# Kernel tuning notes

Hardware: AMD Instinct MI355X
Metric: run time of the kernel (lower is better)

The kernel has to match this reference:

```python
import jax, jax.numpy as jnp
import numpy as np

B = 512; Nt = 8; Nr = 8; Ld = 256; Lp = 16; qAry = 2
LDPC_N = qAry * Nt * Ld      # 4096
M_A = 3 * LDPC_N             # 12288
SQ2 = float(np.sqrt(2.0))


def setup_inputs() -> dict:
    key = jax.random.key(0)
    ks = jax.random.split(key, 12)
    # Sparse-ish binary ADMM expansion matrix A (rows = check-edge constraints)
    A = (jax.random.uniform(ks[0], (M_A, LDPC_N)) < 0.005).astype(jnp.float32)
    # Lambda_A ~ column weights of A (keeps the w denominator well behaved)
    Lambda_A = (jnp.sum(A, axis=0) + 1.0).reshape(LDPC_N, 1)
    theta = jax.random.uniform(ks[1], (M_A, 1), dtype=jnp.float32)
    sigma2_I = jnp.tile(0.1 * jnp.eye(2 * Nt, dtype=jnp.float32)[None], (B, 1, 1))
    return {
        "sigma2_I": sigma2_I,
        "Y": jax.random.normal(ks[2], (B, 2 * Nr, Ld), dtype=jnp.float32),
        "YYp": jax.random.normal(ks[3], (B, Nr, 2 * (Ld + Lp)), dtype=jnp.float32),
        "real_Xp": jax.random.normal(ks[4], (B, Nt, Lp), dtype=jnp.float32) / SQ2,
        "imag_Xp": jax.random.normal(ks[5], (B, Nt, Lp), dtype=jnp.float32) / SQ2,
        "lambda_W": jax.random.uniform(ks[6], (B, 1, 1), minval=0.5, maxval=1.5),
        "F": jax.random.normal(ks[7], (B, 2 * Nt, Ld), dtype=jnp.float32),
        "u": jax.random.uniform(ks[8], (B, LDPC_N, 1), dtype=jnp.float32),
        "z": jax.random.uniform(ks[9], (B, M_A, 1), dtype=jnp.float32),
        "lambda1": jax.random.uniform(ks[10], (B, M_A, 1), dtype=jnp.float32),
        "acc_new": jnp.zeros((B, 1, 1), dtype=jnp.float32),
        "A": A, "theta": theta, "Lambda_A": Lambda_A,
        "miu": jnp.full((1, 1), 0.6, dtype=jnp.float32),
        "alpha": jnp.full((1, 1), 11.0, dtype=jnp.float32),
        "factor": jnp.full((1, 1), 1.0, dtype=jnp.float32),
        "relax": jnp.full((1, 1), 1.0, dtype=jnp.float32),
        "acc": jnp.full((1, 1), 0.0, dtype=jnp.float32),
    }


def reference(sigma2_I, Y, YYp, real_Xp, imag_Xp, lambda_W, F, u, z, lambda1,
              acc_new, A, theta, Lambda_A, miu, alpha, factor, relax, acc):
    relu = jax.nn.relu
    z_old, lam_old = z, lambda1
    A_T = A.T
    # --- qAry == 2 detection update ---
    fb = 4.0 * lambda_W                                   # (B,1,1)
    # reorder F (B, 2Nt, Ld) into bit layout (B, 2*Nt*Ld, 1)
    res = F.transpose(0, 2, 1).reshape(-1, Ld, 2, Nt).transpose(0, 1, 3, 2)
    res = res.reshape(-1, 2 * Nt * Ld, 1)
    fb_res = 2.0 * lambda_W - 2.0 * SQ2 * res
    q = miu * jnp.matmul(A_T, theta - z - lambda1) + fb_res - alpha  # (B,LDPC_N,1)
    w = 1.0 / (miu * Lambda_A + fb - 2.0 * alpha)
    u = q * w
    u = relu(u) - relu(u - 1.0)                           # clip to [0,1]
    u_order = u.reshape(-1, Ld, Nt, qAry).transpose(0, 2, 1, 3)  # (B,Nt,Ld,2)
    real_X = (1.0 - 2.0 * u_order[:, :, :, 0]) / SQ2      # (B,Nt,Ld)
    imag_X = (1.0 - 2.0 * u_order[:, :, :, 1]) / SQ2
    X = jnp.concatenate([real_X, imag_X], axis=1)          # (B,2Nt,Ld)
    # --- MMSE channel re-estimation ---
    real_XXp = jnp.concatenate([real_X, real_Xp], axis=2)
    imag_XXp = jnp.concatenate([imag_X, imag_Xp], axis=2)
    XXp = jnp.concatenate([jnp.concatenate([real_XXp, imag_XXp], 2),
                           jnp.concatenate([-imag_XXp, real_XXp], 2)], 1)  # (B,2Nt,2(Ld+Lp))
    R = jnp.matmul(XXp, XXp.transpose(0, 2, 1)) + sigma2_I  # (B,2Nt,2Nt)
    inv_R = jnp.linalg.inv(R)
    W_temp = jnp.matmul(jnp.matmul(inv_R, XXp), YYp.transpose(0, 2, 1))  # (B,2Nt,Nr)
    real_W = W_temp[:, :Nt, :]
    imag_W = W_temp[:, Nt:2 * Nt, :]
    W = jnp.concatenate([jnp.concatenate([real_W, imag_W], 2),
                         jnp.concatenate([-imag_W, real_W], 2)], 1).transpose(0, 2, 1)  # (B,2Nr,2Nt)
    lambda_W = factor * lambda_W
    WT = W.transpose(0, 2, 1)
    F_new = jnp.matmul(WT, Y) + lambda_W * X - jnp.matmul(jnp.matmul(WT, W), X)
    # --- z / lambda1 ADMM update ---
    ztemp = theta - relax * jnp.matmul(A, u) - (1.0 - relax) * (theta - z_old) - lambda1
    z = relu(ztemp)
    lambda1 = -ztemp + z
    z = z + acc * (z - z_old)
    lambda1 = lambda1 + acc * (lambda1 - lam_old)
    return (lambda_W, F_new, u, z, lambda1, acc_new)
```

## Files before the change

### kernel.cpp

```cpp
#include <hip/hip_runtime.h>
#include <math.h>

#define BB 512
#define NT 8
#define NR 8
#define LDIM 256
#define LP 16
#define LDPC_N 4096
#define M_A 12288
#define COLCAP 128
#define ROWCAP 64
#define K2I 16
#define SQ2 1.41421356237309515f
#define INVSQ2 0.70710678118654752f

typedef unsigned short u16;
typedef unsigned int u32;

__device__ __forceinline__ float bflo(u32 u) { return __uint_as_float(u << 16); }
__device__ __forceinline__ float bfhi(u32 u) { return __uint_as_float(u & 0xffff0000u); }
__device__ __forceinline__ u16 f2bf(float f) {
  u32 b = __float_as_uint(f);
  return (u16)((b + 0x7fffu + ((b >> 16) & 1u)) >> 16);
}

__global__ __launch_bounds__(256) void build_sparse(
    const float* __restrict__ A, int* __restrict__ colcnt, int* __restrict__ rowcnt,
    int* __restrict__ csc_c, int* __restrict__ csr_c) {
  const long long total4 = (long long)M_A * LDPC_N / 4;
  long long stride = (long long)gridDim.x * blockDim.x;
  for (long long t = (long long)blockIdx.x * blockDim.x + threadIdx.x; t < total4; t += stride) {
    float4 a = ((const float4*)A)[t];
    long long base = t * 4;
    float av[4] = {a.x, a.y, a.z, a.w};
#pragma unroll
    for (int l = 0; l < 4; l++) {
      if (av[l] != 0.0f) {
        long long lin = base + l;
        int i = (int)(lin >> 12);
        int j = (int)(lin & 4095);
        int sc = atomicAdd(&colcnt[j], 1);
        if (sc < COLCAP) csc_c[j * COLCAP + sc] = i;
        int sr = atomicAdd(&rowcnt[i], 1);
        if (sr < ROWCAP) csr_c[i * ROWCAP + sr] = j;
      }
    }
  }
}

__global__ __launch_bounds__(256) void t1tf(
    const float* __restrict__ z, const float* __restrict__ lam,
    const float* __restrict__ theta, const float* __restrict__ F,
    u16* __restrict__ VT, u16* __restrict__ FT) {
  __shared__ float tile[256 * 33];
  int bx = blockIdx.x;
  if (bx < 6144) {
    int i0 = (bx % 384) * 32, b0 = (bx / 384) * 32;
    {
      int il = threadIdx.x & 31, bq = threadIdx.x >> 5;
      float th = theta[i0 + il];
#pragma unroll
      for (int m = 0; m < 4; m++) {
        int bl = bq + m * 8;
        size_t off = (size_t)(b0 + bl) * M_A + i0 + il;
        tile[il * 33 + bl] = th - z[off] - lam[off];
      }
    }
    __syncthreads();
    {
      int bl = threadIdx.x & 31, iq = threadIdx.x >> 5;
#pragma unroll
      for (int m = 0; m < 4; m++) {
        int il = iq + m * 8;
        VT[(size_t)(i0 + il) * BB + b0 + bl] = f2bf(tile[il * 33 + bl]);
      }
    }
  } else {
    int t = bx - 6144;
    int j0 = (t & 15) * 256, b0 = (t >> 4) * 32;
    int ld0 = j0 >> 4;
    int cc = threadIdx.x >> 4, dd = threadIdx.x & 15;
    int jl = dd * 16 + ((cc & 7) << 1) + (cc >> 3);
    for (int m = 0; m < 32; m++) {
      tile[jl * 33 + m] = F[(size_t)(b0 + m) * 4096 + cc * 256 + ld0 + dd];
    }
    __syncthreads();
    int bl = threadIdx.x & 31, jq = threadIdx.x >> 5;
    for (int jj = 0; jj < 32; jj++) {
      int jlo = jq * 32 + jj;
      FT[(size_t)(j0 + jlo) * BB + b0 + bl] = f2bf(tile[jlo * 33 + bl]);
    }
  }
}

__global__ __launch_bounds__(256) void k1_spmm(
    const u16* __restrict__ VT, const u16* __restrict__ FT,
    const int* __restrict__ colcnt, const int* __restrict__ csc_c,
    const float* __restrict__ lambda_W, const float* __restrict__ Lambda_A,
    const float* __restrict__ miu_p, const float* __restrict__ alpha_p,
    u16* __restrict__ UT) {
  __shared__ int idx[4 * COLCAP];
  __shared__ int cnts[4];
  __shared__ float lamA[4];
  int j0 = blockIdx.x * 4;
  int t = threadIdx.x;
  for (int s = t; s < 4 * COLCAP; s += 256) idx[s] = csc_c[j0 * COLCAP + s];
  if (t < 4) {
    cnts[t] = min(colcnt[j0 + t], COLCAP);
    lamA[t] = Lambda_A[j0 + t];
  }
  __syncthreads();
  float miu = miu_p[0], alpha = alpha_p[0];
  float2 lw2 = *(const float2*)&lambda_W[2 * t];
#pragma unroll
  for (int c = 0; c < 4; c++) {
    int cnt = cnts[c];
    const int* ic = &idx[c * COLCAP];
    float a0 = 0.0f, a1 = 0.0f;
    int k = 0;
    for (; k + 3 < cnt; k += 4) {
      int4 i4 = *(const int4*)&ic[k];
      u32 w0 = *(const u32*)&VT[(size_t)i4.x * BB + 2 * t];
      u32 w1 = *(const u32*)&VT[(size_t)i4.y * BB + 2 * t];
      u32 w2 = *(const u32*)&VT[(size_t)i4.z * BB + 2 * t];
      u32 w3 = *(const u32*)&VT[(size_t)i4.w * BB + 2 * t];
      a0 += (bflo(w0) + bflo(w1)) + (bflo(w2) + bflo(w3));
      a1 += (bfhi(w0) + bfhi(w1)) + (bfhi(w2) + bfhi(w3));
    }
    for (; k < cnt; k++) {
      u32 w = *(const u32*)&VT[(size_t)ic[k] * BB + 2 * t];
      a0 += bflo(w);
      a1 += bfhi(w);
    }
    int j = j0 + c;
    u32 rr = *(const u32*)&FT[(size_t)j * BB + 2 * t];
    float res0 = bflo(rr), res1 = bfhi(rr);
    float q0 = miu * a0 + 2.0f * lw2.x - 2.0f * SQ2 * res0 - alpha;
    float q1 = miu * a1 + 2.0f * lw2.y - 2.0f * SQ2 * res1 - alpha;
    float w0 = 1.0f / (miu * lamA[c] + 4.0f * lw2.x - 2.0f * alpha);
    float w1 = 1.0f / (miu * lamA[c] + 4.0f * lw2.y - 2.0f * alpha);
    float u0 = fminf(fmaxf(q0 * w0, 0.0f), 1.0f);
    float u1 = fminf(fmaxf(q1 * w1, 0.0f), 1.0f);
    u32 packed = (u32)f2bf(u0) | ((u32)f2bf(u1) << 16);
    *(u32*)&UT[(size_t)j * BB + 2 * t] = packed;
  }
}

__global__ __launch_bounds__(256) void tu_ut(const u16* __restrict__ UT, float* __restrict__ out_u) {
  __shared__ float tile[32 * 33];
  int j0 = blockIdx.x * 32, b0 = blockIdx.y * 32;
  {
    int bl = threadIdx.x & 31, jq = threadIdx.x >> 5;
#pragma unroll
    for (int m = 0; m < 4; m++) {
      int jl = jq + m * 8;
      tile[jl * 33 + bl] = bflo((u32)UT[(size_t)(j0 + jl) * BB + b0 + bl]);
    }
  }
  __syncthreads();
  {
    int jl = threadIdx.x & 31, bq = threadIdx.x >> 5;
#pragma unroll
    for (int m = 0; m < 4; m++) {
      int bl = bq + m * 8;
      out_u[(size_t)(b0 + bl) * LDPC_N + j0 + jl] = tile[jl * 33 + bl];
    }
  }
}

__global__ __launch_bounds__(256) void k2_spmm(
    const u16* __restrict__ UT, const float* __restrict__ z_old,
    const float* __restrict__ lam_old, const float* __restrict__ theta,
    const float* __restrict__ relax_p, const float* __restrict__ acc_p,
    const int* __restrict__ rowcnt, const int* __restrict__ csr_c,
    float* __restrict__ out_z, float* __restrict__ out_lam) {
  __shared__ int idx[K2I * ROWCAP];
  __shared__ int cnts[K2I];
  __shared__ float ths[K2I];
  __shared__ float ssum[K2I * 514];
  int i0 = blockIdx.x * K2I;
  int t = threadIdx.x;
  for (int s = t; s < K2I * ROWCAP; s += 256) idx[s] = csr_c[i0 * ROWCAP + s];
  if (t < K2I) {
    cnts[t] = min(rowcnt[i0 + t], ROWCAP);
    ths[t] = theta[i0 + t];
  }
  __syncthreads();
  for (int r = 0; r < K2I; r++) {
    int cnt = cnts[r];
    const int* ir = &idx[r * ROWCAP];
    float s0 = 0.0f, s1 = 0.0f;
    int k = 0;
    for (; k + 3 < cnt; k += 4) {
      int4 i4 = *(const int4*)&ir[k];
      u32 w0 = *(const u32*)&UT[(size_t)i4.x * BB + 2 * t];
      u32 w1 = *(const u32*)&UT[(size_t)i4.y * BB + 2 * t];
      u32 w2 = *(const u32*)&UT[(size_t)i4.z * BB + 2 * t];
      u32 w3 = *(const u32*)&UT[(size_t)i4.w * BB + 2 * t];
      s0 += (bflo(w0) + bflo(w1)) + (bflo(w2) + bflo(w3));
      s1 += (bfhi(w0) + bfhi(w1)) + (bfhi(w2) + bfhi(w3));
    }
    for (; k < cnt; k++) {
      u32 w = *(const u32*)&UT[(size_t)ir[k] * BB + 2 * t];
      s0 += bflo(w);
      s1 += bfhi(w);
    }
    *(float2*)&ssum[r * 514 + 2 * t] = make_float2(s0, s1);
  }
  __syncthreads();
  float relax = relax_p[0], acc = acc_p[0];
  int iw = t & 15, bq = t >> 4;
  float th = ths[iw];
  for (int p = 0; p < 32; p++) {
    int b = p * 16 + bq;
    size_t off = (size_t)b * M_A + i0 + iw;
    float zo = z_old[off];
    float lo = lam_old[off];
    float s = ssum[iw * 514 + b];
    float ztemp = th - relax * s - (1.0f - relax) * (th - zo) - lo;
    float zn = fmaxf(ztemp, 0.0f);
    float ln = zn - ztemp;
    out_z[off] = zn + acc * (zn - zo);
    out_lam[off] = ln + acc * (ln - lo);
  }
}

#define RL(i, j) Rs[(i) * 17 + (j)]
__global__ __launch_bounds__(256) void k3_mmse(
    const float* __restrict__ u, const float* __restrict__ real_Xp,
    const float* __restrict__ imag_Xp, const float* __restrict__ sigma2_I,
    const float* __restrict__ YYp, const float* __restrict__ Y,
    const float* __restrict__ lambda_W, const float* __restrict__ factor_p,
    const float* __restrict__ acc_new_in,
    float* __restrict__ out_lw, float* __restrict__ out_F, float* __restrict__ out_accnew) {
  __shared__ float XX[16][545];
  __shared__ float yy[8 * 545];
  __shared__ float Rs[16 * 17];
  __shared__ float invd[16];
  __shared__ float Tm[16][8];
  __shared__ float Wcs[256];
  __shared__ float Gs[256];
  int b = blockIdx.x;
  int tid = threadIdx.x;

  const float4* u4 = (const float4*)(u + (size_t)b * LDPC_N);
  for (int m = tid; m < 1024; m += 256) {
    float4 q = u4[m];
    int ld = m >> 2;
    int nt = (2 * m) & 7;
    float vr0 = (1.0f - 2.0f * q.x) * INVSQ2;
    float vi0 = (1.0f - 2.0f * q.y) * INVSQ2;
    float vr1 = (1.0f - 2.0f * q.z) * INVSQ2;
    float vi1 = (1.0f - 2.0f * q.w) * INVSQ2;
    XX[nt][ld] = vr0;        XX[nt][272 + ld] = vi0;
    XX[8 + nt][ld] = -vi0;   XX[8 + nt][272 + ld] = vr0;
    XX[nt + 1][ld] = vr1;    XX[nt + 1][272 + ld] = vi1;
    XX[9 + nt][ld] = -vi1;   XX[9 + nt][272 + ld] = vr1;
  }
  if (tid < 128) {
    int r = tid >> 4, pc = tid & 15;
    float vr = real_Xp[(size_t)b * 128 + tid];
    float vi = imag_Xp[(size_t)b * 128 + tid];
    XX[r][256 + pc] = vr;      XX[r][528 + pc] = vi;
    XX[8 + r][256 + pc] = -vi; XX[8 + r][528 + pc] = vr;
  }
  {
    const float4* y4 = (const float4*)(YYp + (size_t)b * NR * 544);
    for (int s = tid; s < 1088; s += 256) {
      float4 v = y4[s];
      int lin = s * 4;
      int row = lin / 544, col = lin % 544;
      float* d = &yy[row * 545 + col];
      d[0] = v.x; d[1] = v.y; d[2] = v.z; d[3] = v.w;
    }
  }
  __syncthreads();

  for (int p = tid; p < 264; p += 256) {
    if (p < 136) {
      int i = 0;
      while ((i + 1) * (i + 2) / 2 <= p) i++;
      int j = p - i * (i + 1) / 2;
      float s = 0.0f;
      for (int k = 0; k < 544; k++) s += XX[i][k] * XX[j][k];
      RL(i, j) = s + sigma2_I[(size_t)b * 256 + i * 16 + j];
    } else {
      int q = p - 136;
      int i = q >> 3, m = q & 7;
      float s = 0.0f;
      for (int k = 0; k < 544; k++) s += XX[i][k] * yy[m * 545 + k];
      Tm[i][m] = s;
    }
  }
  __syncthreads();

  for (int k = 0; k < 16; k++) {
    if (tid == 0) {
      float d = sqrtf(fmaxf(RL(k, k), 1e-30f));
      RL(k, k) = d;
      invd[k] = 1.0f / d;
    }
    __syncthreads();
    if (tid > k && tid < 16) RL(tid, k) *= invd[k];
    __syncthreads();
    {
      int i = tid >> 4, j = tid & 15;
      if (i > k && j > k && j <= i) RL(i, j) -= RL(i, k) * RL(j, k);
    }
    __syncthreads();
  }

  if (tid < 8) {
    int m = tid;
    float yv[16], wv[16];
#pragma unroll
    for (int r = 0; r < 16; r++) {
      float s = Tm[r][m];
      for (int c = 0; c < r; c++) s -= RL(r, c) * yv[c];
      yv[r] = s * invd[r];
    }
#pragma unroll
    for (int r = 15; r >= 0; r--) {
      float s = yv[r];
      for (int c = r + 1; c < 16; c++) s -= RL(c, r) * wv[c];
      wv[r] = s * invd[r];
    }
#pragma unroll
    for (int r = 0; r < 16; r++) Tm[r][m] = wv[r];
  }
  __syncthreads();

  {
    int i = tid >> 4, j = tid & 15;
    int ii = i & 7, jj = j & 7;
    float val;
    if (i < 8) val = (j < 8) ? Tm[ii][jj] : Tm[8 + ii][jj];
    else       val = (j < 8) ? -Tm[8 + ii][jj] : Tm[ii][jj];
    Wcs[tid] = val;
  }
  __syncthreads();
  {
    int i = tid >> 4, j = tid & 15;
    float s = 0.0f;
#pragma unroll
    for (int k = 0; k < 16; k++) s += Wcs[i * 16 + k] * Wcs[j * 16 + k];
    Gs[tid] = s;
  }
  __syncthreads();

  float lw_new = factor_p[0] * lambda_W[b];
  {
    int ld = tid;
    float Xv[16], Yv[16];
#pragma unroll
    for (int c = 0; c < 8; c++) {
      Xv[c] = XX[c][ld];
      Xv[8 + c] = XX[c][272 + ld];
    }
    const float* Yb = Y + (size_t)b * 16 * LDIM;
#pragma unroll
    for (int c = 0; c < 16; c++) Yv[c] = Yb[c * LDIM + ld];
    float* Fb = out_F + (size_t)b * 16 * LDIM;
    for (int r = 0; r < 16; r++) {
      float s = lw_new * Xv[r];
#pragma unroll
      for (int c = 0; c < 16; c++) s += Wcs[r * 16 + c] * Yv[c] - Gs[r * 16 + c] * Xv[c];
      Fb[r * LDIM + ld] = s;
    }
  }
  if (tid == 0) {
    out_lw[b] = lw_new;
    out_accnew[b] = acc_new_in[b];
  }
}

extern "C" void kernel_launch(void* const* d_in, const int* in_sizes, int n_in,
                              void* d_out, int out_size, void* d_ws, size_t ws_size,
                              hipStream_t stream) {
  const float* sigma2_I  = (const float*)d_in[0];
  const float* Y         = (const float*)d_in[1];
  const float* YYp       = (const float*)d_in[2];
  const float* real_Xp   = (const float*)d_in[3];
  const float* imag_Xp   = (const float*)d_in[4];
  const float* lambda_W  = (const float*)d_in[5];
  const float* F         = (const float*)d_in[6];
  const float* z         = (const float*)d_in[8];
  const float* lam       = (const float*)d_in[9];
  const float* acc_new_i = (const float*)d_in[10];
  const float* A         = (const float*)d_in[11];
  const float* theta     = (const float*)d_in[12];
  const float* Lambda_A  = (const float*)d_in[13];
  const float* miu       = (const float*)d_in[14];
  const float* alpha     = (const float*)d_in[15];
  const float* factor    = (const float*)d_in[16];
  const float* relax     = (const float*)d_in[17];
  const float* acc       = (const float*)d_in[18];

  float* out = (float*)d_out;
  float* out_lw     = out;
  float* out_F      = out_lw + BB;
  float* out_u      = out_F + (size_t)BB * 2 * NT * LDIM;
  float* out_z      = out_u + (size_t)BB * LDPC_N;
  float* out_lam    = out_z + (size_t)BB * M_A;
  float* out_accnew = out_lam + (size_t)BB * M_A;

  u16* VT = (u16*)out_z;
  u16* FT = (u16*)out_lam;
  u16* UT = (u16*)out_F;

  int* ws = (int*)d_ws;
  int* colcnt = ws;
  int* rowcnt = colcnt + LDPC_N;
  int* csc_c  = rowcnt + M_A;
  int* csr_c  = csc_c + COLCAP * LDPC_N;

  hipMemsetAsync(colcnt, 0, (LDPC_N + M_A) * sizeof(int), stream);
  build_sparse<<<2048, 256, 0, stream>>>(A, colcnt, rowcnt, csc_c, csr_c);
  t1tf<<<6400, 256, 0, stream>>>(z, lam, theta, F, VT, FT);
  k1_spmm<<<LDPC_N / 4, 256, 0, stream>>>(VT, FT, colcnt, csc_c, lambda_W,
                                          Lambda_A, miu, alpha, UT);
  tu_ut<<<dim3(LDPC_N / 32, BB / 32), 256, 0, stream>>>(UT, out_u);
  k2_spmm<<<M_A / K2I, 256, 0, stream>>>(UT, z, lam, theta, relax, acc,
                                         rowcnt, csr_c, out_z, out_lam);
  k3_mmse<<<BB, 256, 0, stream>>>(out_u, real_Xp, imag_Xp, sigma2_I, YYp, Y,
                                  lambda_W, factor, acc_new_i,
                                  out_lw, out_F, out_accnew);
}
```

Measured before the change: 508.4 us.

## Merge transpose, z-update and MMSE kernels into one launch; widen SpMM loads

The u-transpose, z/lambda ADMM update and MMSE re-estimation kernels become a single fused launch that dispatches on block index ranges, so the three independent stages can run concurrently. The UT buffer moves into the workspace so the MMSE part no longer waits on out_u. The MMSE blocks now gather u from UT with strided, uncoalesced accesses and read YYp from global memory instead of staging it in shared memory. Both SpMM kernels switch to one wave per column or row with 16-byte loads of 8 batch entries per lane, which gives fewer, wider gathers.

```diff
diff --git a/kernel.cpp b/kernel.cpp
--- a/kernel.cpp
+++ b/kernel.cpp
@@ -10,7 +10,6 @@
 #define M_A 12288
 #define COLCAP 128
 #define ROWCAP 64
-#define K2I 16
 #define SQ2 1.41421356237309515f
 #define INVSQ2 0.70710678118654752f
 
@@ -22,6 +21,12 @@
 __device__ __forceinline__ u16 f2bf(float f) {
   u32 b = __float_as_uint(f);
   return (u16)((b + 0x7fffu + ((b >> 16) & 1u)) >> 16);
+}
+__device__ __forceinline__ void add8(const uint4& v, float* a) {
+  a[0] += bflo(v.x); a[1] += bfhi(v.x);
+  a[2] += bflo(v.y); a[3] += bfhi(v.y);
+  a[4] += bflo(v.z); a[5] += bfhi(v.z);
+  a[6] += bflo(v.w); a[7] += bfhi(v.w);
 }
 
 __global__ __launch_bounds__(256) void build_sparse(
@@ -100,277 +105,272 @@
     const float* __restrict__ miu_p, const float* __restrict__ alpha_p,
     u16* __restrict__ UT) {
   __shared__ int idx[4 * COLCAP];
+  __shared__ float lwS[512];
   __shared__ int cnts[4];
   __shared__ float lamA[4];
   int j0 = blockIdx.x * 4;
   int t = threadIdx.x;
   for (int s = t; s < 4 * COLCAP; s += 256) idx[s] = csc_c[j0 * COLCAP + s];
+  for (int s = t; s < 512; s += 256) lwS[s] = lambda_W[s];
   if (t < 4) {
     cnts[t] = min(colcnt[j0 + t], COLCAP);
     lamA[t] = Lambda_A[j0 + t];
   }
   __syncthreads();
+  int w = t >> 6, l = t & 63;
+  int j = j0 + w;
+  int boff = 8 * l;
+  int cnt = cnts[w];
+  const int* ic = &idx[w * COLCAP];
+  float av[8] = {0, 0, 0, 0, 0, 0, 0, 0};
+  int k = 0;
+  for (; k + 1 < cnt; k += 2) {
+    uint4 va = *(const uint4*)&VT[(size_t)ic[k] * BB + boff];
+    uint4 vb = *(const uint4*)&VT[(size_t)ic[k + 1] * BB + boff];
+    add8(va, av);
+    add8(vb, av);
+  }
+  if (k < cnt) {
+    uint4 va = *(const uint4*)&VT[(size_t)ic[k] * BB + boff];
+    add8(va, av);
+  }
   float miu = miu_p[0], alpha = alpha_p[0];
-  float2 lw2 = *(const float2*)&lambda_W[2 * t];
-#pragma unroll
-  for (int c = 0; c < 4; c++) {
-    int cnt = cnts[c];
-    const int* ic = &idx[c * COLCAP];
-    float a0 = 0.0f, a1 = 0.0f;
-    int k = 0;
-    for (; k + 3 < cnt; k += 4) {
-      int4 i4 = *(const int4*)&ic[k];
-      u32 w0 = *(const u32*)&VT[(size_t)i4.x * BB + 2 * t];
-      u32 w1 = *(const u32*)&VT[(size_t)i4.y * BB + 2 * t];
-      u32 w2 = *(const u32*)&VT[(size_t)i4.z * BB + 2 * t];
-      u32 w3 = *(const u32*)&VT[(size_t)i4.w * BB + 2 * t];
-      a0 += (bflo(w0) + bflo(w1)) + (bflo(w2) + bflo(w3));
-      a1 += (bfhi(w0) + bfhi(w1)) + (bfhi(w2) + bfhi(w3));
-    }
-    for (; k < cnt; k++) {
-      u32 w = *(const u32*)&VT[(size_t)ic[k] * BB + 2 * t];
-      a0 += bflo(w);
-      a1 += bfhi(w);
-    }
-    int j = j0 + c;
-    u32 rr = *(const u32*)&FT[(size_t)j * BB + 2 * t];
-    float res0 = bflo(rr), res1 = bfhi(rr);
-    float q0 = miu * a0 + 2.0f * lw2.x - 2.0f * SQ2 * res0 - alpha;
-    float q1 = miu * a1 + 2.0f * lw2.y - 2.0f * SQ2 * res1 - alpha;
-    float w0 = 1.0f / (miu * lamA[c] + 4.0f * lw2.x - 2.0f * alpha);
-    float w1 = 1.0f / (miu * lamA[c] + 4.0f * lw2.y - 2.0f * alpha);
+  float la = lamA[w];
+  uint4 fr = *(const uint4*)&FT[(size_t)j * BB + boff];
+  float res[8] = {bflo(fr.x), bfhi(fr.x), bflo(fr.y), bfhi(fr.y),
+                  bflo(fr.z), bfhi(fr.z), bflo(fr.w), bfhi(fr.w)};
+  u32 pk[4];
+#pragma unroll
+  for (int e = 0; e < 4; e++) {
+    float lw0 = lwS[boff + 2 * e], lw1 = lwS[boff + 2 * e + 1];
+    float q0 = miu * av[2 * e] + 2.0f * lw0 - 2.0f * SQ2 * res[2 * e] - alpha;
+    float q1 = miu * av[2 * e + 1] + 2.0f * lw1 - 2.0f * SQ2 * res[2 * e + 1] - alpha;
+    float w0 = 1.0f / (miu * la + 4.0f * lw0 - 2.0f * alpha);
+    float w1 = 1.0f / (miu * la + 4.0f * lw1 - 2.0f * alpha);
     float u0 = fminf(fmaxf(q0 * w0, 0.0f), 1.0f);
     float u1 = fminf(fmaxf(q1 * w1, 0.0f), 1.0f);
-    u32 packed = (u32)f2bf(u0) | ((u32)f2bf(u1) << 16);
-    *(u32*)&UT[(size_t)j * BB + 2 * t] = packed;
-  }
-}
-
-__global__ __launch_bounds__(256) void tu_ut(const u16* __restrict__ UT, float* __restrict__ out_u) {
-  __shared__ float tile[32 * 33];
-  int j0 = blockIdx.x * 32, b0 = blockIdx.y * 32;
-  {
-    int bl = threadIdx.x & 31, jq = threadIdx.x >> 5;
-#pragma unroll
-    for (int m = 0; m < 4; m++) {
-      int jl = jq + m * 8;
-      tile[jl * 33 + bl] = bflo((u32)UT[(size_t)(j0 + jl) * BB + b0 + bl]);
-    }
-  }
-  __syncthreads();
-  {
-    int jl = threadIdx.x & 31, bq = threadIdx.x >> 5;
-#pragma unroll
-    for (int m = 0; m < 4; m++) {
-      int bl = bq + m * 8;
-      out_u[(size_t)(b0 + bl) * LDPC_N + j0 + jl] = tile[jl * 33 + bl];
-    }
-  }
-}
-
-__global__ __launch_bounds__(256) void k2_spmm(
+    pk[e] = (u32)f2bf(u0) | ((u32)f2bf(u1) << 16);
+  }
+  *(uint4*)&UT[(size_t)j * BB + boff] = make_uint4(pk[0], pk[1], pk[2], pk[3]);
+}
+
+__global__ __launch_bounds__(256) void fused3(
     const u16* __restrict__ UT, const float* __restrict__ z_old,
     const float* __restrict__ lam_old, const float* __restrict__ theta,
     const float* __restrict__ relax_p, const float* __restrict__ acc_p,
     const int* __restrict__ rowcnt, const int* __restrict__ csr_c,
-    float* __restrict__ out_z, float* __restrict__ out_lam) {
-  __shared__ int idx[K2I * ROWCAP];
-  __shared__ int cnts[K2I];
-  __shared__ float ths[K2I];
-  __shared__ float ssum[K2I * 514];
-  int i0 = blockIdx.x * K2I;
-  int t = threadIdx.x;
-  for (int s = t; s < K2I * ROWCAP; s += 256) idx[s] = csr_c[i0 * ROWCAP + s];
-  if (t < K2I) {
-    cnts[t] = min(rowcnt[i0 + t], ROWCAP);
-    ths[t] = theta[i0 + t];
-  }
-  __syncthreads();
-  for (int r = 0; r < K2I; r++) {
-    int cnt = cnts[r];
-    const int* ir = &idx[r * ROWCAP];
-    float s0 = 0.0f, s1 = 0.0f;
-    int k = 0;
-    for (; k + 3 < cnt; k += 4) {
-      int4 i4 = *(const int4*)&ir[k];
-      u32 w0 = *(const u32*)&UT[(size_t)i4.x * BB + 2 * t];
-      u32 w1 = *(const u32*)&UT[(size_t)i4.y * BB + 2 * t];
-      u32 w2 = *(const u32*)&UT[(size_t)i4.z * BB + 2 * t];
-      u32 w3 = *(const u32*)&UT[(size_t)i4.w * BB + 2 * t];
-      s0 += (bflo(w0) + bflo(w1)) + (bflo(w2) + bflo(w3));
-      s1 += (bfhi(w0) + bfhi(w1)) + (bfhi(w2) + bfhi(w3));
-    }
-    for (; k < cnt; k++) {
-      u32 w = *(const u32*)&UT[(size_t)ir[k] * BB + 2 * t];
-      s0 += bflo(w);
-      s1 += bfhi(w);
-    }
-    *(float2*)&ssum[r * 514 + 2 * t] = make_float2(s0, s1);
-  }
-  __syncthreads();
-  float relax = relax_p[0], acc = acc_p[0];
-  int iw = t & 15, bq = t >> 4;
-  float th = ths[iw];
-  for (int p = 0; p < 32; p++) {
-    int b = p * 16 + bq;
-    size_t off = (size_t)b * M_A + i0 + iw;
-    float zo = z_old[off];
-    float lo = lam_old[off];
-    float s = ssum[iw * 514 + b];
-    float ztemp = th - relax * s - (1.0f - relax) * (th - zo) - lo;
-    float zn = fmaxf(ztemp, 0.0f);
-    float ln = zn - ztemp;
-    out_z[off] = zn + acc * (zn - zo);
-    out_lam[off] = ln + acc * (ln - lo);
-  }
-}
-
-#define RL(i, j) Rs[(i) * 17 + (j)]
-__global__ __launch_bounds__(256) void k3_mmse(
-    const float* __restrict__ u, const float* __restrict__ real_Xp,
-    const float* __restrict__ imag_Xp, const float* __restrict__ sigma2_I,
-    const float* __restrict__ YYp, const float* __restrict__ Y,
-    const float* __restrict__ lambda_W, const float* __restrict__ factor_p,
-    const float* __restrict__ acc_new_in,
+    float* __restrict__ out_u, float* __restrict__ out_z, float* __restrict__ out_lam,
+    const float* __restrict__ real_Xp, const float* __restrict__ imag_Xp,
+    const float* __restrict__ sigma2_I, const float* __restrict__ YYp,
+    const float* __restrict__ Y, const float* __restrict__ lambda_W,
+    const float* __restrict__ factor_p, const float* __restrict__ acc_new_in,
     float* __restrict__ out_lw, float* __restrict__ out_F, float* __restrict__ out_accnew) {
-  __shared__ float XX[16][545];
-  __shared__ float yy[8 * 545];
-  __shared__ float Rs[16 * 17];
-  __shared__ float invd[16];
-  __shared__ float Tm[16][8];
-  __shared__ float Wcs[256];
-  __shared__ float Gs[256];
-  int b = blockIdx.x;
+  __shared__ float smem[9856];
+  int bidx = blockIdx.x;
   int tid = threadIdx.x;
 
-  const float4* u4 = (const float4*)(u + (size_t)b * LDPC_N);
-  for (int m = tid; m < 1024; m += 256) {
-    float4 q = u4[m];
-    int ld = m >> 2;
-    int nt = (2 * m) & 7;
-    float vr0 = (1.0f - 2.0f * q.x) * INVSQ2;
-    float vi0 = (1.0f - 2.0f * q.y) * INVSQ2;
-    float vr1 = (1.0f - 2.0f * q.z) * INVSQ2;
-    float vi1 = (1.0f - 2.0f * q.w) * INVSQ2;
-    XX[nt][ld] = vr0;        XX[nt][272 + ld] = vi0;
-    XX[8 + nt][ld] = -vi0;   XX[8 + nt][272 + ld] = vr0;
-    XX[nt + 1][ld] = vr1;    XX[nt + 1][272 + ld] = vi1;
-    XX[9 + nt][ld] = -vi1;   XX[9 + nt][272 + ld] = vr1;
-  }
-  if (tid < 128) {
-    int r = tid >> 4, pc = tid & 15;
-    float vr = real_Xp[(size_t)b * 128 + tid];
-    float vi = imag_Xp[(size_t)b * 128 + tid];
-    XX[r][256 + pc] = vr;      XX[r][528 + pc] = vi;
-    XX[8 + r][256 + pc] = -vi; XX[8 + r][528 + pc] = vr;
-  }
-  {
-    const float4* y4 = (const float4*)(YYp + (size_t)b * NR * 544);
-    for (int s = tid; s < 1088; s += 256) {
-      float4 v = y4[s];
-      int lin = s * 4;
-      int row = lin / 544, col = lin % 544;
-      float* d = &yy[row * 545 + col];
-      d[0] = v.x; d[1] = v.y; d[2] = v.z; d[3] = v.w;
-    }
-  }
-  __syncthreads();
-
-  for (int p = tid; p < 264; p += 256) {
-    if (p < 136) {
-      int i = 0;
-      while ((i + 1) * (i + 2) / 2 <= p) i++;
-      int j = p - i * (i + 1) / 2;
+  if (bidx < 2048) {
+    float* tile = smem;
+    int j0 = (bidx & 127) * 32, b0 = (bidx >> 7) * 32;
+    {
+      int bl = tid & 31, jq = tid >> 5;
+#pragma unroll
+      for (int m = 0; m < 4; m++) {
+        int jl = jq + m * 8;
+        tile[jl * 33 + bl] = bflo((u32)UT[(size_t)(j0 + jl) * BB + b0 + bl]);
+      }
+    }
+    __syncthreads();
+    {
+      int jl = tid & 31, bq = tid >> 5;
+#pragma unroll
+      for (int m = 0; m < 4; m++) {
+        int bl = bq + m * 8;
+        out_u[(size_t)(b0 + bl) * LDPC_N + j0 + jl] = tile[jl * 33 + bl];
+      }
+    }
+  } else if (bidx < 2816) {
+    int* idx = (int*)smem;
+    int* cnts = idx + 1024;
+    float* ths = (float*)(idx + 1040);
+    float* ssum = (float*)(idx + 1056);
+    int i0 = (bidx - 2048) * 16;
+    for (int s = tid; s < 1024; s += 256) idx[s] = csr_c[i0 * ROWCAP + s];
+    if (tid < 16) {
+      cnts[tid] = min(rowcnt[i0 + tid], ROWCAP);
+      ths[tid] = theta[i0 + tid];
+    }
+    __syncthreads();
+    int w = tid >> 6, l = tid & 63, boff = 8 * l;
+    for (int rr = 0; rr < 4; rr++) {
+      int r = w * 4 + rr;
+      int cnt = cnts[r];
+      const int* ir = &idx[r * ROWCAP];
+      float s[8] = {0, 0, 0, 0, 0, 0, 0, 0};
+      int k = 0;
+      for (; k + 1 < cnt; k += 2) {
+        uint4 va = *(const uint4*)&UT[(size_t)ir[k] * BB + boff];
+        uint4 vb = *(const uint4*)&UT[(size_t)ir[k + 1] * BB + boff];
+        add8(va, s);
+        add8(vb, s);
+      }
+      if (k < cnt) {
+        uint4 va = *(const uint4*)&UT[(size_t)ir[k] * BB + boff];
+        add8(va, s);
+      }
+      *(float4*)&ssum[r * 520 + boff] = make_float4(s[0], s[1], s[2], s[3]);
+      *(float4*)&ssum[r * 520 + boff + 4] = make_float4(s[4], s[5], s[6], s[7]);
+    }
+    __syncthreads();
+    float relax = relax_p[0], acc = acc_p[0];
+    int iw = tid & 15, bq = tid >> 4;
+    float th = ths[iw];
+    for (int p = 0; p < 32; p++) {
+      int b = p * 16 + bq;
+      size_t off = (size_t)b * M_A + i0 + iw;
+      float zo = z_old[off];
+      float lo = lam_old[off];
+      float s = ssum[iw * 520 + b];
+      float ztemp = th - relax * s - (1.0f - relax) * (th - zo) - lo;
+      float zn = fmaxf(ztemp, 0.0f);
+      float ln = zn - ztemp;
+      out_z[off] = zn + acc * (zn - zo);
+      out_lam[off] = ln + acc * (ln - lo);
+    }
+  } else {
+    float* XX = smem;
+    float* Rs = XX + 8720;
+    float* invd = Rs + 272;
+    float* Tm = invd + 16;
+    float* Wcs = Tm + 128;
+    float* Gs = Wcs + 256;
+#define XXA(r, c) XX[(r) * 545 + (c)]
+#define RLp(i, j) Rs[(i) * 17 + (j)]
+    int b = bidx - 2816;
+
+    for (int m = tid; m < 1024; m += 256) {
+      int ld = m >> 2;
+      int nt = (2 * m) & 7;
+      int j4 = 4 * m;
+      float q0 = bflo((u32)UT[(size_t)(j4 + 0) * BB + b]);
+      float q1 = bflo((u32)UT[(size_t)(j4 + 1) * BB + b]);
+      float q2 = bflo((u32)UT[(size_t)(j4 + 2) * BB + b]);
+      float q3 = bflo((u32)UT[(size_t)(j4 + 3) * BB + b]);
+      float vr0 = (1.0f - 2.0f * q0) * INVSQ2, vi0 = (1.0f - 2.0f * q1) * INVSQ2;
+      float vr1 = (1.0f - 2.0f * q2) * INVSQ2, vi1 = (1.0f - 2.0f * q3) * INVSQ2;
+      XXA(nt, ld) = vr0;          XXA(nt, 272 + ld) = vi0;
+      XXA(8 + nt, ld) = -vi0;     XXA(8 + nt, 272 + ld) = vr0;
+      XXA(nt + 1, ld) = vr1;      XXA(nt + 1, 272 + ld) = vi1;
+      XXA(9 + nt, ld) = -vi1;     XXA(9 + nt, 272 + ld) = vr1;
+    }
+    if (tid < 128) {
+      int r = tid >> 4, pc = tid & 15;
+      float vr = real_Xp[(size_t)b * 128 + tid];
+      float vi = imag_Xp[(size_t)b * 128 + tid];
+      XXA(r, 256 + pc) = vr;       XXA(r, 528 + pc) = vi;
+      XXA(8 + r, 256 + pc) = -vi;  XXA(8 + r, 528 + pc) = vr;
+    }
+    __syncthreads();
+
+    for (int p = tid; p < 264; p += 256) {
+      if (p < 136) {
+        int i = 0;
+        while ((i + 1) * (i + 2) / 2 <= p) i++;
+        int jj = p - i * (i + 1) / 2;
+        float s = 0.0f;
+        for (int k = 0; k < 544; k++) s += XXA(i, k) * XXA(jj, k);
+        RLp(i, jj) = s + sigma2_I[(size_t)b * 256 + i * 16 + jj];
+      } else {
+        int q = p - 136;
+        int i = q >> 3, m = q & 7;
+        const float* yb = YYp + (size_t)b * 4352 + m * 544;
+        float s = 0.0f;
+        for (int k = 0; k < 544; k++) s += XXA(i, k) * yb[k];
+        Tm[i * 8 + m] = s;
+      }
+    }
+    __syncthreads();
+
+    for (int k = 0; k < 16; k++) {
+      if (tid == 0) {
+        float d = sqrtf(fmaxf(RLp(k, k), 1e-30f));
+        RLp(k, k) = d;
+        invd[k] = 1.0f / d;
+      }
+      __syncthreads();
+      if (tid > k && tid < 16) RLp(tid, k) *= invd[k];
+      __syncthreads();
+      {
+        int i = tid >> 4, jj = tid & 15;
+        if (i > k && jj > k && jj <= i) RLp(i, jj) -= RLp(i, k) * RLp(jj, k);
+      }
+      __syncthreads();
+    }
+
+    if (tid < 8) {
+      int m = tid;
+      float yv[16], wv[16];
+#pragma unroll
+      for (int r = 0; r < 16; r++) {
+        float s = Tm[r * 8 + m];
+        for (int c = 0; c < r; c++) s -= RLp(r, c) * yv[c];
+        yv[r] = s * invd[r];
+      }
+#pragma unroll
+      for (int r = 15; r >= 0; r--) {
+        float s = yv[r];
+        for (int c = r + 1; c < 16; c++) s -= RLp(c, r) * wv[c];
+        wv[r] = s * invd[r];
+      }
+#pragma unroll
+      for (int r = 0; r < 16; r++) Tm[r * 8 + m] = wv[r];
+    }
+    __syncthreads();
+
+    {
+      int i = tid >> 4, jj = tid & 15;
+      int ii = i & 7, jc = jj & 7;
+      float val;
+      if (i < 8) val = (jj < 8) ? Tm[ii * 8 + jc] : Tm[(8 + ii) * 8 + jc];
+      else       val = (jj < 8) ? -Tm[(8 + ii) * 8 + jc] : Tm[ii * 8 + jc];
+      Wcs[tid] = val;
+    }
+    __syncthreads();
+    {
+      int i = tid >> 4, jj = tid & 15;
       float s = 0.0f;
-      for (int k = 0; k < 544; k++) s += XX[i][k] * XX[j][k];
-      RL(i, j) = s + sigma2_I[(size_t)b * 256 + i * 16 + j];
-    } else {
-      int q = p - 136;
-      int i = q >> 3, m = q & 7;
-      float s = 0.0f;
-      for (int k = 0; k < 544; k++) s += XX[i][k] * yy[m * 545 + k];
-      Tm[i][m] = s;
-    }
-  }
-  __syncthreads();
-
-  for (int k = 0; k < 16; k++) {
+#pragma unroll
+      for (int k = 0; k < 16; k++) s += Wcs[i * 16 + k] * Wcs[jj * 16 + k];
+      Gs[tid] = s;
+    }
+    __syncthreads();
+
+    float lw_new = factor_p[0] * lambda_W[b];
+    {
+      int ld = tid;
+      float Xv[16], Yv[16];
+#pragma unroll
+      for (int c = 0; c < 8; c++) {
+        Xv[c] = XXA(c, ld);
+        Xv[8 + c] = XXA(c, 272 + ld);
+      }
+      const float* Yb = Y + (size_t)b * 16 * LDIM;
+#pragma unroll
+      for (int c = 0; c < 16; c++) Yv[c] = Yb[c * LDIM + ld];
+      float* Fb = out_F + (size_t)b * 16 * LDIM;
+      for (int r = 0; r < 16; r++) {
+        float s = lw_new * Xv[r];
+#pragma unroll
+        for (int c = 0; c < 16; c++) s += Wcs[r * 16 + c] * Yv[c] - Gs[r * 16 + c] * Xv[c];
+        Fb[r * LDIM + ld] = s;
+      }
+    }
     if (tid == 0) {
-      float d = sqrtf(fmaxf(RL(k, k), 1e-30f));
-      RL(k, k) = d;
-      invd[k] = 1.0f / d;
-    }
-    __syncthreads();
-    if (tid > k && tid < 16) RL(tid, k) *= invd[k];
-    __syncthreads();
-    {
-      int i = tid >> 4, j = tid & 15;
-      if (i > k && j > k && j <= i) RL(i, j) -= RL(i, k) * RL(j, k);
-    }
-    __syncthreads();
-  }
-
-  if (tid < 8) {
-    int m = tid;
-    float yv[16], wv[16];
-#pragma unroll
-    for (int r = 0; r < 16; r++) {
-      float s = Tm[r][m];
-      for (int c = 0; c < r; c++) s -= RL(r, c) * yv[c];
-      yv[r] = s * invd[r];
-    }
-#pragma unroll
-    for (int r = 15; r >= 0; r--) {
-      float s = yv[r];
-      for (int c = r + 1; c < 16; c++) s -= RL(c, r) * wv[c];
-      wv[r] = s * invd[r];
-    }
-#pragma unroll
-    for (int r = 0; r < 16; r++) Tm[r][m] = wv[r];
-  }
-  __syncthreads();
-
-  {
-    int i = tid >> 4, j = tid & 15;
-    int ii = i & 7, jj = j & 7;
-    float val;
-    if (i < 8) val = (j < 8) ? Tm[ii][jj] : Tm[8 + ii][jj];
-    else       val = (j < 8) ? -Tm[8 + ii][jj] : Tm[ii][jj];
-    Wcs[tid] = val;
-  }
-  __syncthreads();
-  {
-    int i = tid >> 4, j = tid & 15;
-    float s = 0.0f;
-#pragma unroll
-    for (int k = 0; k < 16; k++) s += Wcs[i * 16 + k] * Wcs[j * 16 + k];
-    Gs[tid] = s;
-  }
-  __syncthreads();
-
-  float lw_new = factor_p[0] * lambda_W[b];
-  {
-    int ld = tid;
-    float Xv[16], Yv[16];
-#pragma unroll
-    for (int c = 0; c < 8; c++) {
-      Xv[c] = XX[c][ld];
-      Xv[8 + c] = XX[c][272 + ld];
-    }
-    const float* Yb = Y + (size_t)b * 16 * LDIM;
-#pragma unroll
-    for (int c = 0; c < 16; c++) Yv[c] = Yb[c * LDIM + ld];
-    float* Fb = out_F + (size_t)b * 16 * LDIM;
-    for (int r = 0; r < 16; r++) {
-      float s = lw_new * Xv[r];
-#pragma unroll
-      for (int c = 0; c < 16; c++) s += Wcs[r * 16 + c] * Yv[c] - Gs[r * 16 + c] * Xv[c];
-      Fb[r * LDIM + ld] = s;
-    }
-  }
-  if (tid == 0) {
-    out_lw[b] = lw_new;
-    out_accnew[b] = acc_new_in[b];
+      out_lw[b] = lw_new;
+      out_accnew[b] = acc_new_in[b];
+    }
+#undef XXA
+#undef RLp
   }
 }
 
@@ -406,23 +406,21 @@
 
   u16* VT = (u16*)out_z;
   u16* FT = (u16*)out_lam;
-  u16* UT = (u16*)out_F;
 
   int* ws = (int*)d_ws;
   int* colcnt = ws;
   int* rowcnt = colcnt + LDPC_N;
   int* csc_c  = rowcnt + M_A;
   int* csr_c  = csc_c + COLCAP * LDPC_N;
+  u16* UT     = (u16*)(csr_c + ROWCAP * M_A);
 
   hipMemsetAsync(colcnt, 0, (LDPC_N + M_A) * sizeof(int), stream);
   build_sparse<<<2048, 256, 0, stream>>>(A, colcnt, rowcnt, csc_c, csr_c);
   t1tf<<<6400, 256, 0, stream>>>(z, lam, theta, F, VT, FT);
   k1_spmm<<<LDPC_N / 4, 256, 0, stream>>>(VT, FT, colcnt, csc_c, lambda_W,
                                           Lambda_A, miu, alpha, UT);
-  tu_ut<<<dim3(LDPC_N / 32, BB / 32), 256, 0, stream>>>(UT, out_u);
-  k2_spmm<<<M_A / K2I, 256, 0, stream>>>(UT, z, lam, theta, relax, acc,
-                                         rowcnt, csr_c, out_z, out_lam);
-  k3_mmse<<<BB, 256, 0, stream>>>(out_u, real_Xp, imag_Xp, sigma2_I, YYp, Y,
-                                  lambda_W, factor, acc_new_i,
-                                  out_lw, out_F, out_accnew);
-}
+  fused3<<<3328, 256, 0, stream>>>(UT, z, lam, theta, relax, acc, rowcnt, csr_c,
+                                   out_u, out_z, out_lam,
+                                   real_Xp, imag_Xp, sigma2_I, YYp, Y, lambda_W,
+                                   factor, acc_new_i, out_lw, out_F, out_accnew);
+}
```

Result: no change. 505.8 us (-0.5%).
